# Performance work log

Measured on AMD Instinct MI355X. Metric: run time of the kernel, lower is better.

Reference implementation:

```python
import jax, jax.numpy as jnp
import numpy as np

DIM = 1024
D_STATE = 64
D_CONV = 4
EXPAND = 2
D_INNER = DIM * EXPAND          # 2048
N_HEADS = D_INNER // 64         # 32
HEAD_DIM = D_INNER // N_HEADS   # 64
B_SZ = 1
SEQ = 1024
D_IN_PROJ = 2 * D_INNER + 2 * D_STATE + N_HEADS  # 4256
EPS = 1e-6


def setup_inputs() -> dict:
    key = jax.random.key(0)
    ks = jax.random.split(key, 9)
    x = jax.random.normal(ks[0], (B_SZ, SEQ, DIM), jnp.float32)
    W_in = jax.random.normal(ks[1], (D_IN_PROJ, DIM), jnp.float32) / np.sqrt(DIM)
    W_conv = jax.random.normal(ks[2], (D_INNER, 1, D_CONV), jnp.float32) / np.sqrt(D_CONV)
    b_conv = 0.01 * jax.random.normal(ks[3], (D_INNER,), jnp.float32)
    # A_log init: log(arange(1..d_state)) broadcast to (h, d, n), as in the module
    A_log = jnp.log(jnp.arange(1, D_STATE + 1, dtype=jnp.float32)) * jnp.ones((N_HEADS, HEAD_DIM, D_STATE), jnp.float32)
    D = jnp.ones((N_HEADS, HEAD_DIM), jnp.float32) + 0.01 * jax.random.normal(ks[4], (N_HEADS, HEAD_DIM), jnp.float32)
    dt_bias = 0.1 * jax.random.normal(ks[5], (N_HEADS,), jnp.float32)
    norm_w = jnp.ones((D_INNER,), jnp.float32) + 0.01 * jax.random.normal(ks[6], (D_INNER,), jnp.float32)
    W_out = jax.random.normal(ks[7], (DIM, D_INNER), jnp.float32) / np.sqrt(D_INNER)
    return {"x": x, "W_in": W_in, "W_conv": W_conv, "b_conv": b_conv,
            "A_log": A_log, "D": D, "dt_bias": dt_bias, "norm_w": norm_w, "W_out": W_out}


def reference(x, W_in, W_conv, b_conv, A_log, D, dt_bias, norm_w, W_out):
    Bsz, L, _ = x.shape
    zxBCdt = x @ W_in.T  # (B, L, D_IN_PROJ)
    z, xin, Bm, Cm, dt = jnp.split(
        zxBCdt,
        [D_INNER, 2 * D_INNER, 2 * D_INNER + D_STATE, 2 * D_INNER + 2 * D_STATE],
        axis=-1)
    # causal depthwise conv1d (padding d_conv-1 then truncate == left-pad d_conv-1)
    xc = jnp.transpose(xin, (0, 2, 1))  # (B, d_inner, L)
    xc = jax.lax.conv_general_dilated(
        xc, W_conv, window_strides=(1,), padding=[(D_CONV - 1, 0)],
        feature_group_count=D_INNER, dimension_numbers=("NCH", "OIH", "NCH"))
    xc = xc + b_conv[None, :, None]
    xin = jax.nn.silu(jnp.transpose(xc, (0, 2, 1)))  # (B, L, d_inner)
    xh = xin.reshape(Bsz, L, N_HEADS, HEAD_DIM)      # (B, L, h, d)

    A = -jnp.exp(A_log)                     # (h, d, n)
    dt = jax.nn.softplus(dt + dt_bias)      # (B, L, h)

    def step(h_state, ins):
        x_t, dt_t, B_t, C_t = ins  # (B,h,d), (B,h), (B,n), (B,n)
        a = jnp.exp(dt_t[:, :, None, None] * A[None])          # (B,h,d,n)
        h_state = a * h_state + B_t[:, None, None, :] * x_t[..., None]
        y_t = jnp.einsum("bhdn,bn->bhd", h_state, C_t)
        return h_state, y_t

    h0 = jnp.zeros((Bsz, N_HEADS, HEAD_DIM, D_STATE), x.dtype)
    xs = (jnp.moveaxis(xh, 1, 0), jnp.moveaxis(dt, 1, 0),
          jnp.moveaxis(Bm, 1, 0), jnp.moveaxis(Cm, 1, 0))
    _, ys = jax.lax.scan(step, h0, xs)
    y = jnp.moveaxis(ys, 0, 1)              # (B, L, h, d)
    y = y + xh * D[None, None]              # skip term
    y = y.reshape(Bsz, L, D_INNER)
    y = y * jax.nn.silu(z)                  # gating
    rms = jnp.sqrt(jnp.mean(y * y, axis=-1, keepdims=True) + EPS)
    y = y / rms * norm_w                    # RMSNorm
    return y @ W_out.T                      # (B, L, dim)
```

## Files before the change

kernel.cpp:

```cpp
#include <hip/hip_runtime.h>

typedef unsigned short u16;
typedef unsigned int u32;
typedef __attribute__((ext_vector_type(8))) short bf16x8;
typedef __attribute__((ext_vector_type(4))) float f32x4;

#define GPTR(p) ((const __attribute__((address_space(1))) void*)(p))
#define SPTR(p) ((__attribute__((address_space(3))) void*)(p))

#define L_SEQ 1024
#define DIM 1024
#define D_INNER 2048
#define D_STATE 64
#define N_HEADS 32
#define NPROJ 4256
#define NPROJ_PAD 4352
#define COL_Z 0
#define COL_X 2048
#define COL_B 4096
#define COL_C 4160
#define COL_DT 4224
#define NCHUNK 32
#define QCH 32

__device__ __forceinline__ u16 f2bf(float f) {
    unsigned int u = __float_as_uint(f);
    u = u + 0x7fffu + ((u >> 16) & 1u);
    return (u16)(u >> 16);
}
__device__ __forceinline__ float bf2f(u16 h) {
    unsigned int u = ((unsigned int)h) << 16;
    return __uint_as_float(u);
}

__global__ __launch_bounds__(256)
void cast_all_kernel(const float* __restrict__ x, const float* __restrict__ W_in,
                     const float* __restrict__ W_out,
                     u16* __restrict__ xb_hi, u16* __restrict__ xb_lo,
                     u16* __restrict__ Winb, u16* __restrict__ Winb_lo,
                     u16* __restrict__ Woutb)
{
    const int b = blockIdx.x;
    if (b < 1024) {
        const int i = (b * 256 + threadIdx.x) * 4;
        const float4 v = *(const float4*)&x[i];
        const float vs[4] = { v.x, v.y, v.z, v.w };
        u16 oh[4], ol[4];
        #pragma unroll
        for (int j = 0; j < 4; ++j) {
            oh[j] = f2bf(vs[j]);
            ol[j] = f2bf(vs[j] - bf2f(oh[j]));
        }
        *(ushort4*)&xb_hi[i] = *(ushort4*)oh;
        *(ushort4*)&xb_lo[i] = *(ushort4*)ol;
    } else if (b < 5376) {
        const int i = ((b - 1024) * 256 + threadIdx.x) * 4;
        float4 v = make_float4(0.f, 0.f, 0.f, 0.f);
        if (i < NPROJ * DIM) v = *(const float4*)&W_in[i];
        u16 o[4] = { f2bf(v.x), f2bf(v.y), f2bf(v.z), f2bf(v.w) };
        *(ushort4*)&Winb[i] = *(ushort4*)o;
    } else if (b < 5632) {
        const int i = ((b - 5376) * 256 + threadIdx.x) * 4;
        float4 v = make_float4(0.f, 0.f, 0.f, 0.f);
        if (i < (NPROJ - 4096) * DIM) v = *(const float4*)&W_in[(size_t)4096 * DIM + i];
        const float vs[4] = { v.x, v.y, v.z, v.w };
        u16 oh[4], ol[4];
        #pragma unroll
        for (int j = 0; j < 4; ++j) {
            oh[j] = f2bf(vs[j]);
            ol[j] = f2bf(vs[j] - bf2f(oh[j]));
        }
        *(ushort4*)&Winb[(size_t)4096 * DIM + i] = *(ushort4*)oh;
        *(ushort4*)&Winb_lo[i] = *(ushort4*)ol;
    } else {
        const int i = ((b - 5632) * 256 + threadIdx.x) * 4;
        const float4 v = *(const float4*)&W_out[i];
        u16 o[4] = { f2bf(v.x), f2bf(v.y), f2bf(v.z), f2bf(v.w) };
        *(ushort4*)&Woutb[i] = *(ushort4*)o;
    }
}

__global__ __launch_bounds__(256, 2)
void gemm_bt64(const u16* __restrict__ Ah, const u16* __restrict__ Al,
               const u16* __restrict__ Bh, const u16* __restrict__ Bl,
               float* __restrict__ C, int K, int ldc, int precise_from)
{
    __shared__ u16 As[2][64 * 64];
    __shared__ u16 Bs[2][64 * 64];
    const int tid  = threadIdx.x;
    const int wave = tid >> 6;
    const int lane = tid & 63;
    const int row0 = blockIdx.y * 64;
    const int col0 = blockIdx.x * 64;
    const int wm = (wave >> 1) * 32;
    const int wn = (wave & 1) * 32;
    const bool precise = ((int)blockIdx.x >= precise_from);

    f32x4 acc[2][2] = {};

    const int r15 = lane & 15;
    const int q4  = lane >> 4;

    const int reps = precise ? 3 : 1;
    const int nt = K / 64;
    const int total = nt * reps;

    auto stage = [&](int buf, int it) {
        const int kt = (it / reps) * 64;
        const int sub = it - (it / reps) * reps;
        const u16* Asrc = (sub == 2) ? Al : Ah;
        const u16* Bsrc = (sub == 1) ? Bl : Bh;
        #pragma unroll
        for (int call = 0; call < 2; ++call) {
            const int ob = call * 4096 + tid * 16;
            const int row = ob >> 7;
            const int chk = (ob >> 4) & 7;
            const int sch = chk ^ (row & 7);
            const int gk = kt + sch * 8;
            const int lofs = (call * 4096 + wave * 1024) >> 1;
            __builtin_amdgcn_global_load_lds(GPTR(Asrc + (size_t)(row0 + row) * K + gk),
                                             SPTR(&As[buf][lofs]), 16, 0, 0);
            __builtin_amdgcn_global_load_lds(GPTR(Bsrc + (size_t)(col0 + row) * K + gk),
                                             SPTR(&Bs[buf][lofs]), 16, 0, 0);
        }
    };

    stage(0, 0);
    __syncthreads();
    int cur = 0;
    for (int it = 0; it < total; ++it) {
        if (it + 1 < total) stage(cur ^ 1, it + 1);
        #pragma unroll
        for (int s = 0; s < 2; ++s) {
            const int cbase = s * 4 + q4;
            bf16x8 av[2], bv[2];
            #pragma unroll
            for (int i = 0; i < 2; ++i) {
                const int r = wm + i * 16 + r15;
                av[i] = *(const bf16x8*)&As[cur][r * 64 + ((cbase ^ (r & 7)) * 8)];
            }
            #pragma unroll
            for (int j = 0; j < 2; ++j) {
                const int r = wn + j * 16 + r15;
                bv[j] = *(const bf16x8*)&Bs[cur][r * 64 + ((cbase ^ (r & 7)) * 8)];
            }
            #pragma unroll
            for (int i = 0; i < 2; ++i)
                #pragma unroll
                for (int j = 0; j < 2; ++j)
                    acc[i][j] = __builtin_amdgcn_mfma_f32_16x16x32_bf16(av[i], bv[j], acc[i][j], 0, 0, 0);
        }
        __syncthreads();
        cur ^= 1;
    }

    const int cl = lane & 15;
    const int rg = (lane >> 4) * 4;
    #pragma unroll
    for (int i = 0; i < 2; ++i)
        #pragma unroll
        for (int j = 0; j < 2; ++j)
            #pragma unroll
            for (int reg = 0; reg < 4; ++reg) {
                const int rrow = row0 + wm + i * 16 + rg + reg;
                const int ccol = col0 + wn + j * 16 + cl;
                C[(size_t)rrow * ldc + ccol] = acc[i][j][reg];
            }
}

__global__ __launch_bounds__(256, 2)
void gemm_bt128_sk(const u16* __restrict__ Ah, const u16* __restrict__ Bh,
                   float* __restrict__ Cpart, int Kslice, int lda, int ldb, int ldc)
{
    __shared__ u16 As[2][128 * 32];
    __shared__ u16 Bs[2][128 * 32];
    const int tid  = threadIdx.x;
    const int wave = tid >> 6;
    const int lane = tid & 63;
    const int row0 = blockIdx.y * 128;
    const int col0 = blockIdx.x * 128;
    const int wm = (wave >> 1) * 64;
    const int wn = (wave & 1) * 64;
    const int kbase = blockIdx.z * Kslice;
    float* Cp = Cpart + (size_t)blockIdx.z * (1024 * 1024);

    f32x4 acc[4][4] = {};
    const int r15 = lane & 15;
    const int ko  = (lane >> 4) * 8;

    auto stage = [&](int buf, int kt) {
        #pragma unroll
        for (int call = 0; call < 2; ++call) {
            const int ob = call * 4096 + wave * 1024 + lane * 16;
            const int rr = ob >> 6;
            const int kk = (ob & 63) >> 1;
            const int lofs = call * 2048 + wave * 512;
            __builtin_amdgcn_global_load_lds(GPTR(Ah + (size_t)(row0 + rr) * lda + kt + kk),
                                             SPTR(&As[buf][lofs]), 16, 0, 0);
            __builtin_amdgcn_global_load_lds(GPTR(Bh + (size_t)(col0 + rr) * ldb + kt + kk),
                                             SPTR(&Bs[buf][lofs]), 16, 0, 0);
        }
    };

    stage(0, kbase);
    __syncthreads();
    int cur = 0;
    const int nt = Kslice / 32;
    for (int it = 0; it < nt; ++it) {
        if (it + 1 < nt) stage(cur ^ 1, kbase + (it + 1) * 32);
        bf16x8 av[4], bv[4];
        #pragma unroll
        for (int i = 0; i < 4; ++i)
            av[i] = *(const bf16x8*)&As[cur][(wm + i * 16 + r15) * 32 + ko];
        #pragma unroll
        for (int j = 0; j < 4; ++j)
            bv[j] = *(const bf16x8*)&Bs[cur][(wn + j * 16 + r15) * 32 + ko];
        #pragma unroll
        for (int i = 0; i < 4; ++i)
            #pragma unroll
            for (int j = 0; j < 4; ++j)
                acc[i][j] = __builtin_amdgcn_mfma_f32_16x16x32_bf16(av[i], bv[j], acc[i][j], 0, 0, 0);
        __syncthreads();
        cur ^= 1;
    }

    const int cl = lane & 15;
    const int rg = (lane >> 4) * 4;
    #pragma unroll
    for (int i = 0; i < 4; ++i)
        #pragma unroll
        for (int j = 0; j < 4; ++j)
            #pragma unroll
            for (int reg = 0; reg < 4; ++reg)
                Cp[(size_t)(row0 + wm + i * 16 + rg + reg) * ldc + col0 + wn + j * 16 + cl]
                    = acc[i][j][reg];
}

__global__ __launch_bounds__(256)
void reduce4_kernel(const float* __restrict__ Cpart, float* __restrict__ out)
{
    const int i = (blockIdx.x * 256 + threadIdx.x) * 4;
    const float4 a = *(const float4*)&Cpart[i];
    const float4 b = *(const float4*)&Cpart[i + 1024 * 1024];
    const float4 c = *(const float4*)&Cpart[i + 2 * 1024 * 1024];
    const float4 d = *(const float4*)&Cpart[i + 3 * 1024 * 1024];
    *(float4*)&out[i] = make_float4(a.x + b.x + c.x + d.x, a.y + b.y + c.y + d.y,
                                    a.z + b.z + c.z + d.z, a.w + b.w + c.w + d.w);
}

__global__ __launch_bounds__(256)
void conv_dt_kernel(const float* __restrict__ P,
                    const float* __restrict__ Wc,
                    const float* __restrict__ bc,
                    const float* __restrict__ dtb,
                    const float* __restrict__ A_log,
                    float* __restrict__ xconv,
                    float* __restrict__ xT,
                    float2* __restrict__ BCp2,
                    float* __restrict__ gT,
                    float* __restrict__ decayT)
{
    const int b = blockIdx.x;
    if (b < 256) {
        __shared__ float xls[64][33];
        const int tid = threadIdx.x;
        const int t0 = (b & 31) * 32;
        const int c0 = (b >> 5) * 256;
        const int c = c0 + tid;
        const float w0c = Wc[c * 4 + 0], w1c = Wc[c * 4 + 1];
        const float w2c = Wc[c * 4 + 2], w3c = Wc[c * 4 + 3];
        const float bcv = bc[c];
        float w0 = (t0 >= 3) ? P[(size_t)(t0 - 3) * NPROJ_PAD + COL_X + c] : 0.f;
        float w1 = (t0 >= 2) ? P[(size_t)(t0 - 2) * NPROJ_PAD + COL_X + c] : 0.f;
        float w2 = (t0 >= 1) ? P[(size_t)(t0 - 1) * NPROJ_PAD + COL_X + c] : 0.f;
        float o[32];
        #pragma unroll 8
        for (int tl = 0; tl < 32; ++tl) {
            const int t = t0 + tl;
            const float w3 = P[(size_t)t * NPROJ_PAD + COL_X + c];
            float acc = bcv;
            acc = fmaf(w0, w0c, acc);
            acc = fmaf(w1, w1c, acc);
            acc = fmaf(w2, w2c, acc);
            acc = fmaf(w3, w3c, acc);
            const float v = acc / (1.f + __expf(-acc));
            o[tl] = v;
            xconv[(size_t)t * D_INNER + c] = v;
            w0 = w1; w1 = w2; w2 = w3;
        }
        #pragma unroll
        for (int r = 0; r < 2; ++r) {
            __syncthreads();
            const int half = tid >> 7;
            if ((tid >> 6) == r * 2 || (tid >> 6) == r * 2 + 1) {
            }
            if ((tid >> 6) == r * 2) {
                #pragma unroll
                for (int tl = 0; tl < 32; ++tl) xls[tid & 63][tl] = o[tl];
            } else if ((tid >> 6) == r * 2 + 1) {
            }
            __syncthreads();
            {
                const int row = tid >> 2;
                const int qd  = (tid & 3) * 8;
                float4 v0, v1;
                v0.x = xls[row][qd + 0]; v0.y = xls[row][qd + 1];
                v0.z = xls[row][qd + 2]; v0.w = xls[row][qd + 3];
                v1.x = xls[row][qd + 4]; v1.y = xls[row][qd + 5];
                v1.z = xls[row][qd + 6]; v1.w = xls[row][qd + 7];
                float* dst = xT + (size_t)(c0 + r * 128 + row) * L_SEQ + t0 + qd;
                *(float4*)dst = v0;
                *(float4*)(dst + 4) = v1;
            }
            __syncthreads();
            if ((tid >> 6) == r * 2 + 1) {
                #pragma unroll
                for (int tl = 0; tl < 32; ++tl) xls[tid & 63][tl] = o[tl];
            }
            __syncthreads();
            {
                const int row = tid >> 2;
                const int qd  = (tid & 3) * 8;
                float4 v0, v1;
                v0.x = xls[row][qd + 0]; v0.y = xls[row][qd + 1];
                v0.z = xls[row][qd + 2]; v0.w = xls[row][qd + 3];
                v1.x = xls[row][qd + 4]; v1.y = xls[row][qd + 5];
                v1.z = xls[row][qd + 6]; v1.w = xls[row][qd + 7];
                float* dst = xT + (size_t)(c0 + r * 128 + 64 + row) * L_SEQ + t0 + qd;
                *(float4*)dst = v0;
                *(float4*)(dst + 4) = v1;
            }
        }
    } else {
        const int b2 = b - 256;
        const int tid = threadIdx.x;
        #pragma unroll
        for (int e = tid; e < 512; e += 256) {
            const int t = b2 * 8 + (e >> 6);
            const int n = e & 63;
            const float Bv = P[(size_t)t * NPROJ_PAD + COL_B + n];
            const float Cv = P[(size_t)t * NPROJ_PAD + COL_C + n];
            BCp2[t * 64 + n] = make_float2(Bv, Cv);
        }
        const int wv = tid >> 6;
        const int lane = tid & 63;
        const int idx = b2 * 4 + wv;
        const int h = idx >> 4;
        const int pr = idx & 15;
        const int t0 = pr * 64;
        float v = P[(size_t)(t0 + lane) * NPROJ_PAD + COL_DT + h] + dtb[h];
        v = (v > 15.f) ? v : __logf(1.f + __expf(v));
        float g = v;
        #pragma unroll
        for (int off = 1; off < 32; off <<= 1) {
            const float u = __shfl_up(g, off);
            if ((lane & 31) >= off) g += u;
        }
        gT[h * L_SEQ + t0 + lane] = g;
        const float Av = -__expf(A_log[(size_t)h * 4096 + lane]);
        #pragma unroll 8
        for (int tt = 0; tt < 64; ++tt) {
            const float dtt = __shfl(v, tt);
            decayT[((size_t)h * L_SEQ + t0 + tt) * 64 + lane] = __expf(dtt * Av);
        }
    }
}

__global__ __launch_bounds__(128, 2)
void scan_local_kernel(const float2* __restrict__ BCp2,
                       const float* __restrict__ decayT,
                       const float* __restrict__ xT,
                       float* __restrict__ ygt,
                       u16* __restrict__ S)
{
    __shared__ float2 pt[2][2][8][65];
    const int wv = threadIdx.x >> 6;
    const int lane = threadIdx.x & 63;
    const int hd0 = blockIdx.x * 16;
    const int chunk = blockIdx.y * 2 + wv;
    const int h = hd0 >> 6;
    const int tb = chunk * QCH;

    float s[16];
    #pragma unroll
    for (int d = 0; d < 16; ++d) s[d] = 0.f;

    const float2* bc = BCp2 + (size_t)tb * 64 + lane;
    const float* dp = decayT + ((size_t)h * L_SEQ + tb) * 64 + lane;
    const float* xr0 = xT + (size_t)hd0 * L_SEQ + tb;

    const int r16 = lane & 15;
    const int seg = lane >> 4;
    const int rdd = r16 >> 1;
    const int ri  = r16 & 1;

    #pragma unroll
    for (int g = 0; g < 8; ++g) {
        float xv[16][4];
        #pragma unroll
        for (int d = 0; d < 16; ++d) {
            const float4 a = *(const float4*)(xr0 + d * L_SEQ + g * 4);
            xv[d][0]=a.x; xv[d][1]=a.y; xv[d][2]=a.z; xv[d][3]=a.w;
        }
        #pragma unroll
        for (int half = 0; half < 2; ++half) {
            #pragma unroll
            for (int ii2 = 0; ii2 < 2; ++ii2) {
                const int ii = half * 2 + ii2;
                const int i = g * 4 + ii;
                const float2 v = bc[i * 64];
                const float a = dp[i * 64];
                #pragma unroll
                for (int d = 0; d < 16; ++d)
                    s[d] = fmaf(a, s[d], v.x * xv[d][ii]);
                #pragma unroll
                for (int dd = 0; dd < 8; ++dd)
                    pt[wv][ii2][dd][lane] = make_float2(s[2*dd] * v.y, s[2*dd+1] * v.y);
            }
            float px = 0.f, py = 0.f;
            #pragma unroll
            for (int k = 0; k < 16; ++k) {
                const float2 vv = pt[wv][ri][rdd][seg * 16 + k];
                px += vv.x; py += vv.y;
            }
            px += __shfl_xor(px, 16); py += __shfl_xor(py, 16);
            px += __shfl_xor(px, 32); py += __shfl_xor(py, 32);
            if (lane < 16) {
                const int tA = tb + g * 4 + half * 2 + ri;
                *(float2*)&ygt[(size_t)tA * D_INNER + hd0 + 2 * rdd] = make_float2(px, py);
            }
        }
    }
    #pragma unroll
    for (int d = 0; d < 16; ++d)
        S[((size_t)(hd0 + d) * NCHUNK + chunk) * 64 + lane] = f2bf(s[d]);
}

__global__ __launch_bounds__(256)
void chunk_combine_kernel(const float* __restrict__ A_log,
                          const float* __restrict__ gT,
                          u16* __restrict__ S)
{
    const int tid = blockIdx.x * 256 + threadIdx.x;
    const int hd = tid >> 6;
    const int n  = tid & 63;
    const int h  = hd >> 6;
    const float Av = -__expf(A_log[(size_t)hd * 64 + n]);
    float H = 0.f;
    #pragma unroll 8
    for (int c = 0; c < NCHUNK; ++c) {
        const float Gc = gT[h * L_SEQ + c * QCH + QCH - 1];
        const size_t idx = ((size_t)hd * NCHUNK + c) * 64 + n;
        const float Sl = bf2f(S[idx]);
        S[idx] = f2bf(H);
        H = __expf(Av * Gc) * H + Sl;
    }
}

__global__ __launch_bounds__(256, 2)
void scan_cross_mfma(const float* __restrict__ P,
                     const float* __restrict__ gT,
                     const float* __restrict__ A_log,
                     const u16* __restrict__ S,
                     float* __restrict__ ygt)
{
    const int wv = threadIdx.x >> 6;
    const int lane = threadIdx.x & 63;
    const int idx = blockIdx.x * 4 + wv;
    const int h = idx >> 5;
    const int c = idx & 31;
    const int t0 = c * QCH;
    const int l15 = lane & 15;
    const int lk  = (lane >> 4) * 8;

    float Av8[2][8];
    #pragma unroll
    for (int ss = 0; ss < 2; ++ss)
        #pragma unroll
        for (int qq = 0; qq < 8; ++qq)
            Av8[ss][qq] = -__expf(A_log[(size_t)h * 4096 + ss * 32 + lk + qq]);

    bf16x8 fH[4][2];
    #pragma unroll
    for (int i = 0; i < 4; ++i)
        #pragma unroll
        for (int ss = 0; ss < 2; ++ss)
            fH[i][ss] = *(const bf16x8*)&S[((size_t)(h * 64 + i * 16 + l15) * NCHUNK + c) * 64 + ss * 32 + lk];

    bf16x8 fC[2][2];
    #pragma unroll
    for (int j = 0; j < 2; ++j) {
        const int t = t0 + j * 16 + l15;
        const float g = gT[h * L_SEQ + t];
        #pragma unroll
        for (int ss = 0; ss < 2; ++ss) {
            const float* src = P + (size_t)t * NPROJ_PAD + COL_C + ss * 32 + lk;
            const float4 a = *(const float4*)src;
            const float4 b = *(const float4*)(src + 4);
            const float v[8] = { a.x, a.y, a.z, a.w, b.x, b.y, b.z, b.w };
            bf16x8 rr;
            #pragma unroll
            for (int qq = 0; qq < 8; ++qq)
                rr[qq] = (short)f2bf(v[qq] * __expf(Av8[ss][qq] * g));
            fC[j][ss] = rr;
        }
    }

    f32x4 acc[2][4] = {};
    #pragma unroll
    for (int ss = 0; ss < 2; ++ss)
        #pragma unroll
        for (int j = 0; j < 2; ++j)
            #pragma unroll
            for (int i = 0; i < 4; ++i)
                acc[j][i] = __builtin_amdgcn_mfma_f32_16x16x32_bf16(fC[j][ss], fH[i][ss], acc[j][i], 0, 0, 0);

    const int rg = (lane >> 4) * 4;
    #pragma unroll
    for (int j = 0; j < 2; ++j)
        #pragma unroll
        for (int i = 0; i < 4; ++i)
            #pragma unroll
            for (int rr = 0; rr < 4; ++rr) {
                const int t = t0 + j * 16 + rg + rr;
                const int d = h * 64 + i * 16 + l15;
                ygt[(size_t)t * D_INNER + d] += acc[j][i][rr];
            }
}

__global__ __launch_bounds__(256)
void rmsnorm_kernel(const float* __restrict__ ygt,
                    const float* __restrict__ P,
                    const float* __restrict__ xconv,
                    const float* __restrict__ Dp,
                    const float* __restrict__ nw,
                    u16* __restrict__ Yb)
{
    __shared__ float red[4];
    const int t = blockIdx.x;
    const int tid = threadIdx.x;
    const int c0 = tid * 8;
    const float* zrow = P + (size_t)t * NPROJ_PAD + COL_Z + c0;
    const float4 z0 = *(const float4*)zrow;
    const float4 z1 = *(const float4*)(zrow + 4);
    const float zz[8] = { z0.x, z0.y, z0.z, z0.w, z1.x, z1.y, z1.z, z1.w };
    const float* xrow = xconv + (size_t)t * D_INNER + c0;
    const float4 x0 = *(const float4*)xrow;
    const float4 x1 = *(const float4*)(xrow + 4);
    const float xx[8] = { x0.x, x0.y, x0.z, x0.w, x1.x, x1.y, x1.z, x1.w };
    const float4 d0 = *(const float4*)&Dp[c0];
    const float4 d1 = *(const float4*)&Dp[c0 + 4];
    const float dd[8] = { d0.x, d0.y, d0.z, d0.w, d1.x, d1.y, d1.z, d1.w };
    const float* yrow = ygt + (size_t)t * D_INNER + c0;
    const float4 y0 = *(const float4*)yrow;
    const float4 y1 = *(const float4*)(yrow + 4);
    const float yy[8] = { y0.x, y0.y, y0.z, y0.w, y1.x, y1.y, y1.z, y1.w };
    float v[8];
    float ss = 0.f;
    #pragma unroll
    for (int j = 0; j < 8; ++j) {
        const float yv = yy[j] + dd[j] * xx[j];
        const float z = zz[j];
        const float gated = yv * (z / (1.f + __expf(-z)));
        v[j] = gated;
        ss += gated * gated;
    }
    #pragma unroll
    for (int off = 32; off > 0; off >>= 1) ss += __shfl_xor(ss, off);
    const int wave = tid >> 6;
    if ((tid & 63) == 0) red[wave] = ss;
    __syncthreads();
    const float total = red[0] + red[1] + red[2] + red[3];
    const float scale = rsqrtf(total * (1.f / D_INNER) + 1e-6f);
    u16 o[8];
    #pragma unroll
    for (int j = 0; j < 8; ++j)
        o[j] = f2bf(v[j] * scale * nw[c0 + j]);
    *(uint4*)&Yb[(size_t)t * D_INNER + c0] = *(uint4*)o;
}

extern "C" void kernel_launch(void* const* d_in, const int* in_sizes, int n_in,
                              void* d_out, int out_size, void* d_ws, size_t ws_size,
                              hipStream_t stream)
{
    const float* x      = (const float*)d_in[0];
    const float* W_in   = (const float*)d_in[1];
    const float* W_conv = (const float*)d_in[2];
    const float* b_conv = (const float*)d_in[3];
    const float* A_log  = (const float*)d_in[4];
    const float* Dp     = (const float*)d_in[5];
    const float* dt_bias= (const float*)d_in[6];
    const float* norm_w = (const float*)d_in[7];
    const float* W_out  = (const float*)d_in[8];
    float* out = (float*)d_out;

    char* w = (char*)d_ws;
    u16*   xb_hi  = (u16*)(w);
    u16*   xb_lo  = (u16*)(w + (2u  << 20));
    u16*   Winb   = (u16*)(w + (4u  << 20));
    u16*   Winb_lo= (u16*)(w + (12u << 20) + (512u << 10));
    float* decayT = (float*)(w);
    u16*   Yb     = (u16*)(w);
    u16*   S      = (u16*)(w + (8u  << 20));
    u16*   Woutb  = (u16*)(w + (16u << 20));
    float* P      = (float*)(w + (20u << 20));
    float* Cpart  = (float*)(w + (20u << 20));
    float* xconv  = (float*)(w + (37u << 20));
    float* gT     = (float*)(w + (45u << 20));
    float2* BCp2  = (float2*)(w + (45u << 20) + (512u << 10));
    float* ygt    = (float*)(w + (46u << 20));
    float* xT     = (float*)(w + (54u << 20));

    const u16* Winb_lo_virt = Winb_lo - (size_t)4096 * DIM;

    cast_all_kernel<<<dim3(7680), 256, 0, stream>>>(
        x, W_in, W_out, xb_hi, xb_lo, Winb, Winb_lo, Woutb);

    gemm_bt64<<<dim3(NPROJ_PAD / 64, L_SEQ / 64), 256, 0, stream>>>(
        xb_hi, xb_lo, Winb, Winb_lo_virt, P, DIM, NPROJ_PAD, 64);

    conv_dt_kernel<<<dim3(256 + 128), 256, 0, stream>>>(
        P, W_conv, b_conv, dt_bias, A_log, xconv, xT, BCp2, gT, decayT);

    scan_local_kernel<<<dim3(D_INNER / 16, 16), 128, 0, stream>>>(
        BCp2, decayT, xT, ygt, S);
    chunk_combine_kernel<<<dim3(D_INNER * 64 / 256), 256, 0, stream>>>(A_log, gT, S);
    scan_cross_mfma<<<dim3(N_HEADS * NCHUNK / 4), 256, 0, stream>>>(P, gT, A_log, S, ygt);

    rmsnorm_kernel<<<dim3(L_SEQ), 256, 0, stream>>>(ygt, P, xconv, Dp, norm_w, Yb);

    gemm_bt128_sk<<<dim3(DIM / 128, L_SEQ / 128, 4), 256, 0, stream>>>(
        Yb, Woutb, Cpart, D_INNER / 4, D_INNER, D_INNER, DIM);
    reduce4_kernel<<<dim3(DIM * L_SEQ / 4 / 256), 256, 0, stream>>>(Cpart, out);
}
```

Measured before the change: 132.4 us.

## Triple-buffer GEMM LDS staging with explicit vmcnt waits and raw barriers

Both bf16 MFMA GEMM kernels move from double to triple LDS buffering. Two tiles are prefetched ahead, and __syncthreads is replaced by s_waitcnt vmcnt(N) plus s_barrier, so the loop waits only for the oldest tile's global_load_lds. The aim is to hide more global-memory latency behind the MFMA work. The cost is 50% more LDS per block, which may reduce occupancy, and correctness now depends on hand-counted outstanding loads (4 per stage). Some dead code in the conv/transpose kernel is also removed.

```diff
diff --git a/kernel.cpp b/kernel.cpp
--- a/kernel.cpp
+++ b/kernel.cpp
@@ -85,8 +85,8 @@
                const u16* __restrict__ Bh, const u16* __restrict__ Bl,
                float* __restrict__ C, int K, int ldc, int precise_from)
 {
-    __shared__ u16 As[2][64 * 64];
-    __shared__ u16 Bs[2][64 * 64];
+    __shared__ u16 As[3][64 * 64];
+    __shared__ u16 Bs[3][64 * 64];
     const int tid  = threadIdx.x;
     const int wave = tid >> 6;
     const int lane = tid & 63;
@@ -126,10 +126,14 @@
     };
 
     stage(0, 0);
-    __syncthreads();
+    if (total > 1) stage(1, 1);
+    if (total > 2) stage(2, 2);
     int cur = 0;
     for (int it = 0; it < total; ++it) {
-        if (it + 1 < total) stage(cur ^ 1, it + 1);
+        if (it + 2 < total)      asm volatile("s_waitcnt vmcnt(8)" ::: "memory");
+        else if (it + 1 < total) asm volatile("s_waitcnt vmcnt(4)" ::: "memory");
+        else                     asm volatile("s_waitcnt vmcnt(0)" ::: "memory");
+        __builtin_amdgcn_s_barrier();
         #pragma unroll
         for (int s = 0; s < 2; ++s) {
             const int cbase = s * 4 + q4;
@@ -150,8 +154,9 @@
                 for (int j = 0; j < 2; ++j)
                     acc[i][j] = __builtin_amdgcn_mfma_f32_16x16x32_bf16(av[i], bv[j], acc[i][j], 0, 0, 0);
         }
-        __syncthreads();
-        cur ^= 1;
+        __builtin_amdgcn_s_barrier();
+        if (it + 3 < total) stage(cur, it + 3);
+        cur = (cur == 2) ? 0 : cur + 1;
     }
 
     const int cl = lane & 15;
@@ -172,8 +177,8 @@
 void gemm_bt128_sk(const u16* __restrict__ Ah, const u16* __restrict__ Bh,
                    float* __restrict__ Cpart, int Kslice, int lda, int ldb, int ldc)
 {
-    __shared__ u16 As[2][128 * 32];
-    __shared__ u16 Bs[2][128 * 32];
+    __shared__ u16 As[3][128 * 32];
+    __shared__ u16 Bs[3][128 * 32];
     const int tid  = threadIdx.x;
     const int wave = tid >> 6;
     const int lane = tid & 63;
@@ -202,12 +207,16 @@
         }
     };
 
+    const int nt = Kslice / 32;
     stage(0, kbase);
-    __syncthreads();
+    if (nt > 1) stage(1, kbase + 32);
+    if (nt > 2) stage(2, kbase + 64);
     int cur = 0;
-    const int nt = Kslice / 32;
     for (int it = 0; it < nt; ++it) {
-        if (it + 1 < nt) stage(cur ^ 1, kbase + (it + 1) * 32);
+        if (it + 2 < nt)      asm volatile("s_waitcnt vmcnt(8)" ::: "memory");
+        else if (it + 1 < nt) asm volatile("s_waitcnt vmcnt(4)" ::: "memory");
+        else                  asm volatile("s_waitcnt vmcnt(0)" ::: "memory");
+        __builtin_amdgcn_s_barrier();
         bf16x8 av[4], bv[4];
         #pragma unroll
         for (int i = 0; i < 4; ++i)
@@ -220,8 +229,9 @@
             #pragma unroll
             for (int j = 0; j < 4; ++j)
                 acc[i][j] = __builtin_amdgcn_mfma_f32_16x16x32_bf16(av[i], bv[j], acc[i][j], 0, 0, 0);
-        __syncthreads();
-        cur ^= 1;
+        __builtin_amdgcn_s_barrier();
+        if (it + 3 < nt) stage(cur, kbase + (it + 3) * 32);
+        cur = (cur == 2) ? 0 : cur + 1;
     }
 
     const int cl = lane & 15;
@@ -291,13 +301,9 @@
         #pragma unroll
         for (int r = 0; r < 2; ++r) {
             __syncthreads();
-            const int half = tid >> 7;
-            if ((tid >> 6) == r * 2 || (tid >> 6) == r * 2 + 1) {
-            }
             if ((tid >> 6) == r * 2) {
                 #pragma unroll
                 for (int tl = 0; tl < 32; ++tl) xls[tid & 63][tl] = o[tl];
-            } else if ((tid >> 6) == r * 2 + 1) {
             }
             __syncthreads();
             {
```

Result: slower. 136.4 us (+3.0%).
